# Kernel optimization log

Hardware: AMD Instinct MI355X
Metric: run time of the kernel (lower is better)

## Reference

```python
import jax, jax.numpy as jnp
import numpy as np

B = 262144
N_MAX = 4
N_EXPERTS = sum(n * n for n in range(1, N_MAX + 1))  # 30
# offset of expert block for each n (experts within n indexed by l*l + l + m)
OFFSETS = np.cumsum([0] + [n * n for n in range(1, N_MAX)])  # [0,1,5,14]


def _expert_id(n, l, m):
    off = jnp.asarray(OFFSETS, dtype=jnp.int32)
    return off[n - 1] + l * l + l + m  # (B,) int


def setup_inputs() -> dict:
    key = jax.random.key(0)
    ks = jax.random.split(key, 12)
    x = jax.random.normal(ks[0], (B, 3), dtype=jnp.float32)
    # valid coupled quantum numbers: 1<=n<=4, 0<=l<n, -l<=m<=l
    n = jax.random.randint(ks[1], (B,), 1, N_MAX + 1)
    ul = jax.random.uniform(ks[2], (B,))
    l = jnp.floor(ul * n.astype(jnp.float32)).astype(jnp.int32)
    l = jnp.clip(l, 0, n - 1)
    um = jax.random.uniform(ks[3], (B,))
    m = jnp.floor(um * (2 * l + 1).astype(jnp.float32)).astype(jnp.int32) - l
    m = jnp.clip(m, -l, l)
    s = 0.1
    W0 = jax.random.normal(ks[4], (3, 128), dtype=jnp.float32) * s
    b0 = jnp.zeros((128,), dtype=jnp.float32)
    W1 = jax.random.normal(ks[5], (128, 64), dtype=jnp.float32) * s
    b1 = jnp.zeros((64,), dtype=jnp.float32)
    Wa = jax.random.normal(ks[6], (N_EXPERTS, 64, 32), dtype=jnp.float32) * s
    ba = jax.random.normal(ks[7], (N_EXPERTS, 32), dtype=jnp.float32) * s
    Wb = jax.random.normal(ks[8], (N_EXPERTS, 32, 2), dtype=jnp.float32) * s
    bb = jax.random.normal(ks[9], (N_EXPERTS, 2), dtype=jnp.float32) * s
    return {"x": x, "n": n.astype(jnp.int32), "l": l, "m": m,
            "W0": W0, "b0": b0, "W1": W1, "b1": b1,
            "Wa": Wa, "ba": ba, "Wb": Wb, "bb": bb}


def reference(x, n, l, m, W0, b0, W1, b1, Wa, ba, Wb, bb):
    eid = _expert_id(n, l, m)  # (B,)
    # shared trunk (dropout is identity in eval mode)
    h = jnp.tanh(x @ W0 + b0)          # (B,128)
    h = jnp.tanh(h @ W1 + b1)          # (B,64)
    # per-sample expert dispatch via irregular gather of tiny MLP weights
    g = jnp.tanh(jnp.einsum('bd,bdh->bh', h, Wa[eid]) + ba[eid])  # (B,32)
    psi = jnp.einsum('bh,bho->bo', g, Wb[eid]) + bb[eid]          # (B,2)
    norm = jnp.sqrt(jnp.sum(psi * psi, axis=1, keepdims=True) + 1e-6)
    return psi / norm
```

## Files before the change

### kernel.cpp

```cpp
#include <hip/hip_runtime.h>
#include <math.h>


#define THREADS 256
#define NE 30
#define HB 128
#define MAXBLK 1056
#define SA 259
#define SG 36

typedef short bf16x8 __attribute__((ext_vector_type(8)));
typedef float f32x4 __attribute__((ext_vector_type(4)));

__device__ __forceinline__ int expert_id(int nn, int ll, int mm) {
    return ((nn - 1) * nn * (2 * nn - 1)) / 6 + ll * ll + ll + mm;
}

__device__ __forceinline__ float fast_tanh(float v) {
    float e = __builtin_exp2f(v * 2.885390082f);
    return fmaf(-2.0f, __builtin_amdgcn_rcpf(e + 1.0f), 1.0f);
}

__device__ __forceinline__ unsigned int f2b(float f) {
    unsigned int u = __float_as_uint(f);
    return (u + 0x7fffu + ((u >> 16) & 1u)) >> 16;
}
__device__ __forceinline__ float b2f(unsigned int b) {
    return __uint_as_float(b << 16);
}
__device__ __forceinline__ unsigned int packsplit(float v) {
    const unsigned int hb = f2b(v);
    const float lo = v - b2f(hb);
    return (__float_as_uint(lo) & 0xffff0000u) | hb;
}

union U8 { unsigned int u[4]; bf16x8 v; };
__device__ __forceinline__ void unpack8(const unsigned int* w, bf16x8& hi, bf16x8& lo) {
    U8 H, L;
#pragma unroll
    for (int i = 0; i < 4; ++i) {
        H.u[i] = __builtin_amdgcn_perm(w[2 * i + 1], w[2 * i], 0x05040100u);
        L.u[i] = __builtin_amdgcn_perm(w[2 * i + 1], w[2 * i], 0x07060302u);
    }
    hi = H.v; lo = L.v;
}

__global__ void hist_pack_kernel(const int* __restrict__ nq, const int* __restrict__ lq,
                                 const int* __restrict__ mq,
                                 int* __restrict__ eids, int* __restrict__ etot,
                                 int* __restrict__ bbase,
                                 const float* __restrict__ W1,
                                 unsigned short* __restrict__ W1fh, unsigned short* __restrict__ W1fl,
                                 const float* __restrict__ Wa,
                                 unsigned short* __restrict__ Wafh, unsigned short* __restrict__ Wafl,
                                 int B) {
    const int tid = threadIdx.x;
    const int bx = blockIdx.x;
    if (bx < HB) {
        __shared__ int h[NE];
        if (tid < NE) h[tid] = 0;
        __syncthreads();
        const int per = B / HB, base = bx * per;
        for (int i = tid; i < per; i += blockDim.x) {
            const int e = expert_id(nq[base + i], lq[base + i], mq[base + i]);
            eids[base + i] = e;
            atomicAdd(&h[e], 1);
        }
        __syncthreads();
        if (tid < NE) bbase[bx * NE + tid] = atomicAdd(&etot[tid], h[tid]);
    } else if (bx == HB) {
        for (int i = tid; i < 8192; i += blockDim.x) {
            const int j = i & 7, s = (i >> 3) & 15, q = (i >> 7) & 3;
            const int nt = (i >> 9) & 3, c = i >> 11;
            const int k = c * 32 + q * 8 + j, n = nt * 16 + s;
            const float w = W1[k * 64 + n];
            const unsigned int hb = f2b(w);
            W1fh[i] = (unsigned short)hb;
            W1fl[i] = (unsigned short)f2b(w - b2f(hb));
        }
    } else {
        const int e = bx - HB - 1;
        for (int i = tid; i < 2048; i += blockDim.x) {
            const int j = i & 7, s = (i >> 3) & 15, q = (i >> 7) & 3;
            const int nt2 = (i >> 9) & 1, c2 = (i >> 10) & 1;
            const int d = c2 * 32 + q * 8 + j, hh = nt2 * 16 + s;
            const float w = Wa[e * 2048 + d * 32 + hh];
            const unsigned int hb = f2b(w);
            Wafh[e * 2048 + i] = (unsigned short)hb;
            Wafl[e * 2048 + i] = (unsigned short)f2b(w - b2f(hb));
        }
    }
}

__global__ void scatter_kernel(const int* __restrict__ eids, const int* __restrict__ etot,
                               const int* __restrict__ bbase, int* __restrict__ perm, int B) {
    __shared__ int lcnt[NE], esrt[NE], bb[NE];
    const int tid = threadIdx.x;
    if (tid < NE) { lcnt[tid] = 0; bb[tid] = bbase[blockIdx.x * NE + tid]; }
    if (tid == 0) {
        int es = 0;
        for (int e = 0; e < NE; ++e) { esrt[e] = es; es += etot[e]; }
    }
    __syncthreads();
    const int per = B / gridDim.x;
    const int blk = blockIdx.x * per;
    for (int i = tid; i < per; i += blockDim.x) {
        const int idx = blk + i;
        const int e = eids[idx];
        const int r = atomicAdd(&lcnt[e], 1);
        perm[esrt[e] + bb[e] + r] = idx;
    }
}

__global__ __launch_bounds__(THREADS, 3) void wfc_kernel(
    const float* __restrict__ x, const int* __restrict__ perm,
    const int* __restrict__ etot,
    const float* __restrict__ W0, const float* __restrict__ b0,
    const bf16x8* __restrict__ W1fh, const bf16x8* __restrict__ W1fl,
    const float* __restrict__ b1,
    const bf16x8* __restrict__ Wafh, const bf16x8* __restrict__ Wafl,
    const float* __restrict__ ba,
    const float* __restrict__ Wb, const float* __restrict__ bb,
    float* __restrict__ out)
{
    __shared__ unsigned int sbuf[9216];

    int eid = -1, start = 0, cnt = 0;
    {
        int cum = 0, es = 0;
#pragma unroll 1
        for (int e = 0; e < NE; ++e) {
            const int t = etot[e];
            const int nb = (t + THREADS - 1) >> 8;
            if ((int)blockIdx.x < cum + nb) {
                const int seg = blockIdx.x - cum;
                eid = e; start = es + seg * THREADS; cnt = min(THREADS, t - seg * THREADS);
                break;
            }
            cum += nb; es += t;
        }
    }
    if (eid < 0) return;
    eid = __builtin_amdgcn_readfirstlane(eid);

    const int tid = threadIdx.x;
    const bool valid = tid < cnt;
    const int idx = perm[start + (valid ? tid : 0)];

    const int lane = tid & 63;
    const int wv   = tid >> 6;
    const int qd   = lane >> 4;
    const int l16  = lane & 15;

    const float x0 = x[idx * 3 + 0];
    const float x1 = x[idx * 3 + 1];
    const float x2 = x[idx * 3 + 2];

    f32x4 acc[4][4];
#pragma unroll
    for (int nt = 0; nt < 4; ++nt) {
        const float bv = b1[nt * 16 + l16];
#pragma unroll
        for (int mt = 0; mt < 4; ++mt) {
            f32x4 c; c[0] = bv; c[1] = bv; c[2] = bv; c[3] = bv;
            acc[mt][nt] = c;
        }
    }

    for (int c = 0; c < 4; ++c) {
        if (c) __syncthreads();
#pragma unroll
        for (int kk = 0; kk < 32; ++kk) {
            const int k = c * 32 + kk;
            const float pre = fmaf(x0, W0[k], fmaf(x1, W0[128 + k], fmaf(x2, W0[256 + k], b0[k])));
            sbuf[kk * SA + tid] = packsplit(fast_tanh(pre));
        }
        __syncthreads();

        bf16x8 Bhi[4], Blo[4];
#pragma unroll
        for (int nt = 0; nt < 4; ++nt) {
            const int rec = (c * 4 + nt) * 64 + qd * 16 + l16;
            Bhi[nt] = W1fh[rec];
            Blo[nt] = W1fl[rec];
        }
#pragma unroll
        for (int mt = 0; mt < 4; ++mt) {
            unsigned int a[8];
            const int mrow = wv * 64 + mt * 16 + l16;
#pragma unroll
            for (int j = 0; j < 8; ++j) a[j] = sbuf[(qd * 8 + j) * SA + mrow];
            bf16x8 Ahi, Alo;
            unpack8(a, Ahi, Alo);
#pragma unroll
            for (int nt = 0; nt < 4; ++nt) {
                acc[mt][nt] = __builtin_amdgcn_mfma_f32_16x16x32_bf16(Ahi, Bhi[nt], acc[mt][nt], 0, 0, 0);
                acc[mt][nt] = __builtin_amdgcn_mfma_f32_16x16x32_bf16(Ahi, Blo[nt], acc[mt][nt], 0, 0, 0);
                acc[mt][nt] = __builtin_amdgcn_mfma_f32_16x16x32_bf16(Alo, Bhi[nt], acc[mt][nt], 0, 0, 0);
            }
        }
    }

    f32x4 acc2[4][2];
#pragma unroll
    for (int nt2 = 0; nt2 < 2; ++nt2) {
        const float bv = ba[(eid << 5) + nt2 * 16 + l16];
#pragma unroll
        for (int mt = 0; mt < 4; ++mt) {
            f32x4 c; c[0] = bv; c[1] = bv; c[2] = bv; c[3] = bv;
            acc2[mt][nt2] = c;
        }
    }

    const bf16x8* __restrict__ waeh = Wafh + (eid << 8);
    const bf16x8* __restrict__ wael = Wafl + (eid << 8);
    for (int c2 = 0; c2 < 2; ++c2) {
        __syncthreads();
#pragma unroll
        for (int mt = 0; mt < 4; ++mt) {
#pragma unroll
            for (int ntl = 0; ntl < 2; ++ntl) {
#pragma unroll
                for (int r = 0; r < 4; ++r) {
                    const float h2 = fast_tanh(acc[mt][c2 * 2 + ntl][r]);
                    const int dl  = ntl * 16 + l16;
                    const int row = wv * 64 + mt * 16 + qd * 4 + r;
                    sbuf[dl * SA + row] = packsplit(h2);
                }
            }
        }
        __syncthreads();

        bf16x8 B2hi[2], B2lo[2];
#pragma unroll
        for (int nt2 = 0; nt2 < 2; ++nt2) {
            const int rec = (c2 * 2 + nt2) * 64 + qd * 16 + l16;
            B2hi[nt2] = waeh[rec];
            B2lo[nt2] = wael[rec];
        }
#pragma unroll
        for (int mt = 0; mt < 4; ++mt) {
            unsigned int a[8];
            const int mrow = wv * 64 + mt * 16 + l16;
#pragma unroll
            for (int j = 0; j < 8; ++j) a[j] = sbuf[(qd * 8 + j) * SA + mrow];
            bf16x8 Ahi, Alo;
            unpack8(a, Ahi, Alo);
#pragma unroll
            for (int nt2 = 0; nt2 < 2; ++nt2) {
                acc2[mt][nt2] = __builtin_amdgcn_mfma_f32_16x16x32_bf16(Ahi, B2hi[nt2], acc2[mt][nt2], 0, 0, 0);
                acc2[mt][nt2] = __builtin_amdgcn_mfma_f32_16x16x32_bf16(Ahi, B2lo[nt2], acc2[mt][nt2], 0, 0, 0);
                acc2[mt][nt2] = __builtin_amdgcn_mfma_f32_16x16x32_bf16(Alo, B2hi[nt2], acc2[mt][nt2], 0, 0, 0);
            }
        }
    }

    __syncthreads();
    float* g2 = (float*)sbuf;
#pragma unroll
    for (int mt = 0; mt < 4; ++mt) {
#pragma unroll
        for (int nt2 = 0; nt2 < 2; ++nt2) {
#pragma unroll
            for (int r = 0; r < 4; ++r) {
                const int row = wv * 64 + mt * 16 + qd * 4 + r;
                g2[row * SG + nt2 * 16 + l16] = fast_tanh(acc2[mt][nt2][r]);
            }
        }
    }
    __syncthreads();

    float gv[32];
    {
        const float4* grow = (const float4*)(g2 + tid * SG);
#pragma unroll
        for (int i = 0; i < 8; ++i) {
            float4 v = grow[i];
            gv[4 * i + 0] = v.x; gv[4 * i + 1] = v.y;
            gv[4 * i + 2] = v.z; gv[4 * i + 3] = v.w;
        }
    }

    const float* __restrict__ wbe = Wb + (eid << 6);
    float p0 = bb[2 * eid], p1 = bb[2 * eid + 1];
#pragma unroll
    for (int h = 0; h < 32; ++h) {
        p0 = fmaf(gv[h], wbe[2 * h + 0], p0);
        p1 = fmaf(gv[h], wbe[2 * h + 1], p1);
    }

    const float s = fmaf(p0, p0, fmaf(p1, p1, 1e-6f));
    const float inv = 1.0f / sqrtf(s);
    if (valid) {
        float2 o; o.x = p0 * inv; o.y = p1 * inv;
        ((float2*)out)[idx] = o;
    }
}

extern "C" void kernel_launch(void* const* d_in, const int* in_sizes, int n_in,
                              void* d_out, int out_size, void* d_ws, size_t ws_size,
                              hipStream_t stream) {
    const float* x  = (const float*)d_in[0];
    const int*   n  = (const int*)d_in[1];
    const int*   l  = (const int*)d_in[2];
    const int*   m  = (const int*)d_in[3];
    const float* W0 = (const float*)d_in[4];
    const float* b0 = (const float*)d_in[5];
    const float* W1 = (const float*)d_in[6];
    const float* b1 = (const float*)d_in[7];
    const float* Wa = (const float*)d_in[8];
    const float* ba = (const float*)d_in[9];
    const float* Wb = (const float*)d_in[10];
    const float* bb = (const float*)d_in[11];
    float* out = (float*)d_out;

    const int B = in_sizes[1];

    int*            perm  = (int*)d_ws;
    int*            eids  = perm + B;
    int*            bbase = eids + B;
    int*            etot  = bbase + HB * NE;
    unsigned short* W1fh  = (unsigned short*)(etot + 32);
    unsigned short* W1fl  = W1fh + 8192;
    unsigned short* Wafh  = W1fl + 8192;
    unsigned short* Wafl  = Wafh + NE * 2048;

    hipMemsetAsync(etot, 0, 32 * sizeof(int), stream);
    hist_pack_kernel<<<HB + 1 + NE, 256, 0, stream>>>(
        n, l, m, eids, etot, bbase, W1, W1fh, W1fl, Wa, Wafh, Wafl, B);
    scatter_kernel<<<HB, 256, 0, stream>>>(eids, etot, bbase, perm, B);
    wfc_kernel<<<MAXBLK, THREADS, 0, stream>>>(
        x, perm, etot, W0, b0,
        (const bf16x8*)W1fh, (const bf16x8*)W1fl, b1,
        (const bf16x8*)Wafh, (const bf16x8*)Wafl, ba, Wb, bb, out);
}
```

Baseline: 141.8 us.

## Shrink compute blocks to one wave, precompute block descriptors, widen histogram grid

Drops the main compute kernel from 256 to 64 threads per block, so each block handles 64 samples of one expert. That cuts padding waste at expert boundaries and lowers shared memory per block, allowing more resident blocks. The per-block linear search over expert totals is replaced by a descriptor table that an extra block in the scatter kernel fills in. The histogram/scatter grid grows from 128 to 1024 blocks for more parallelism, at the cost of a larger per-block base table and more blocks launched.

```diff
diff --git a/kernel.cpp b/kernel.cpp
--- a/kernel.cpp
+++ b/kernel.cpp
@@ -2,11 +2,11 @@
 #include <math.h>
 
 
-#define THREADS 256
+#define THREADS 64
 #define NE 30
-#define HB 128
-#define MAXBLK 1056
-#define SA 259
+#define HB 1024
+#define MAXBLK 4126
+#define SA 67
 #define SG 36
 
 typedef short bf16x8 __attribute__((ext_vector_type(8)));
@@ -93,16 +93,45 @@
 }
 
 __global__ void scatter_kernel(const int* __restrict__ eids, const int* __restrict__ etot,
-                               const int* __restrict__ bbase, int* __restrict__ perm, int B) {
+                               const int* __restrict__ bbase, int* __restrict__ perm,
+                               int4* __restrict__ desc, int B) {
+    const int tid = threadIdx.x;
+    if (blockIdx.x == HB) {
+        __shared__ int es[NE], tq[NE], pb[NE + 1];
+        if (tid == 0) {
+            int e0 = 0, c = 0;
+            for (int e = 0; e < NE; ++e) {
+                const int t = etot[e];
+                es[e] = e0; tq[e] = t; pb[e] = c;
+                c += (t + THREADS - 1) >> 6;
+                e0 += t;
+            }
+            pb[NE] = c;
+        }
+        __syncthreads();
+        const int tot = pb[NE];
+        for (int b = tid; b < MAXBLK; b += blockDim.x) {
+            int4 d = make_int4(-1, 0, 0, 0);
+            if (b < tot) {
+                int e = 0;
+                while (pb[e + 1] <= b) ++e;
+                const int seg = b - pb[e];
+                d.x = e;
+                d.y = es[e] + (seg << 6);
+                d.z = min(THREADS, tq[e] - (seg << 6));
+            }
+            desc[b] = d;
+        }
+        return;
+    }
     __shared__ int lcnt[NE], esrt[NE], bb[NE];
-    const int tid = threadIdx.x;
     if (tid < NE) { lcnt[tid] = 0; bb[tid] = bbase[blockIdx.x * NE + tid]; }
     if (tid == 0) {
-        int es = 0;
-        for (int e = 0; e < NE; ++e) { esrt[e] = es; es += etot[e]; }
+        int es0 = 0;
+        for (int e = 0; e < NE; ++e) { esrt[e] = es0; es0 += etot[e]; }
     }
     __syncthreads();
-    const int per = B / gridDim.x;
+    const int per = B / HB;
     const int blk = blockIdx.x * per;
     for (int i = tid; i < per; i += blockDim.x) {
         const int idx = blk + i;
@@ -112,9 +141,9 @@
     }
 }
 
-__global__ __launch_bounds__(THREADS, 3) void wfc_kernel(
+__global__ __launch_bounds__(THREADS, 4) void wfc_kernel(
     const float* __restrict__ x, const int* __restrict__ perm,
-    const int* __restrict__ etot,
+    const int4* __restrict__ desc,
     const float* __restrict__ W0, const float* __restrict__ b0,
     const bf16x8* __restrict__ W1fh, const bf16x8* __restrict__ W1fl,
     const float* __restrict__ b1,
@@ -123,25 +152,13 @@
     const float* __restrict__ Wb, const float* __restrict__ bb,
     float* __restrict__ out)
 {
-    __shared__ unsigned int sbuf[9216];
-
-    int eid = -1, start = 0, cnt = 0;
-    {
-        int cum = 0, es = 0;
-#pragma unroll 1
-        for (int e = 0; e < NE; ++e) {
-            const int t = etot[e];
-            const int nb = (t + THREADS - 1) >> 8;
-            if ((int)blockIdx.x < cum + nb) {
-                const int seg = blockIdx.x - cum;
-                eid = e; start = es + seg * THREADS; cnt = min(THREADS, t - seg * THREADS);
-                break;
-            }
-            cum += nb; es += t;
-        }
-    }
-    if (eid < 0) return;
-    eid = __builtin_amdgcn_readfirstlane(eid);
+    __shared__ unsigned int sbuf[2304];
+
+    const int4 dsc = desc[blockIdx.x];
+    if (dsc.x < 0) return;
+    const int eid  = __builtin_amdgcn_readfirstlane(dsc.x);
+    const int start = dsc.y;
+    const int cnt   = dsc.z;
 
     const int tid = threadIdx.x;
     const bool valid = tid < cnt;
@@ -320,7 +337,8 @@
     int*            eids  = perm + B;
     int*            bbase = eids + B;
     int*            etot  = bbase + HB * NE;
-    unsigned short* W1fh  = (unsigned short*)(etot + 32);
+    int4*           desc  = (int4*)(etot + 32);
+    unsigned short* W1fh  = (unsigned short*)(desc + MAXBLK);
     unsigned short* W1fl  = W1fh + 8192;
     unsigned short* Wafh  = W1fl + 8192;
     unsigned short* Wafl  = Wafh + NE * 2048;
@@ -328,9 +346,9 @@
     hipMemsetAsync(etot, 0, 32 * sizeof(int), stream);
     hist_pack_kernel<<<HB + 1 + NE, 256, 0, stream>>>(
         n, l, m, eids, etot, bbase, W1, W1fh, W1fl, Wa, Wafh, Wafl, B);
-    scatter_kernel<<<HB, 256, 0, stream>>>(eids, etot, bbase, perm, B);
+    scatter_kernel<<<HB + 1, 256, 0, stream>>>(eids, etot, bbase, perm, desc, B);
     wfc_kernel<<<MAXBLK, THREADS, 0, stream>>>(
-        x, perm, etot, W0, b0,
+        x, perm, desc, W0, b0,
         (const bf16x8*)W1fh, (const bf16x8*)W1fl, b1,
         (const bf16x8*)Wafh, (const bf16x8*)Wafl, ba, Wb, bb, out);
 }
```

Result: slower. 155.8 us (+9.8%).
